# Kernel tuning notes

Hardware: AMD Instinct MI355X
Metric: run time of the kernel (lower is better)

## Reference

```python
import jax, jax.numpy as jnp
import numpy as np

K = 20          # neighbors
EPS = 1e-5      # BatchNorm eps
SLOPE = 0.2     # LeakyReLU negative slope


def setup_inputs() -> dict:
    key = jax.random.key(0)
    k1, k2 = jax.random.split(key)
    B, C, N, O = 8, 64, 4096, 64
    x = jax.random.normal(k1, (B, C, N), dtype=jnp.float32)
    # 1x1 Conv2d(2C -> O, bias=False) kernel, squeezed to (O, 2C)
    W = jax.random.normal(k2, (O, 2 * C), dtype=jnp.float32) * 0.05
    gamma = jnp.ones((O,), jnp.float32)   # BN weight
    beta = jnp.zeros((O,), jnp.float32)   # BN bias
    return {"x": x, "W": W, "gamma": gamma, "beta": beta}


def _edgeconv(x, W, gamma, beta):
    B, C, N = x.shape
    xt = jnp.transpose(x, (0, 2, 1))                       # (B, N, C)
    # KNN on negative squared distance (matches torch topk of -dist)
    xx = jnp.sum(x * x, axis=1)                            # (B, N)
    inner = jnp.einsum('bnc,bmc->bnm', xt, xt)             # (B, N, N)
    neg_dist = 2.0 * inner - xx[:, :, None] - xx[:, None, :]
    _, idx = jax.lax.top_k(neg_dist, K)                    # (B, N, K) int32
    # gather neighbor features: nbr[b,n,k,c] = xt[b, idx[b,n,k], c]
    nbr = xt[jnp.arange(B)[:, None, None], idx]            # (B, N, K, C)
    center = jnp.broadcast_to(xt[:, :, None, :], (B, N, K, C))
    edge = jnp.concatenate([nbr - center, center], axis=-1)  # (B, N, K, 2C)
    # 1x1 conv == channel matmul
    y = jnp.einsum('bnkc,oc->bnko', edge, W)               # (B, N, K, O)
    # BatchNorm2d (training mode: batch statistics over B,N,K per channel)
    mean = jnp.mean(y, axis=(0, 1, 2))
    var = jnp.var(y, axis=(0, 1, 2))
    yn = (y - mean) * jax.lax.rsqrt(var + EPS) * gamma + beta
    ya = jnp.where(yn >= 0, yn, SLOPE * yn)                # LeakyReLU(0.2)
    out = jnp.max(ya, axis=2)                              # max over k -> (B, N, O)
    return jnp.transpose(out, (0, 2, 1))                   # (B, O, N)


def reference(x, W, gamma, beta):
    return _edgeconv(x, W, gamma, beta)
```

## Files before the change

### kernel.cpp

```cpp
#include <hip/hip_runtime.h>
#include <hip/hip_bf16.h>
#include <math.h>

#define B 8
#define C 64
#define NN 4096
#define O 64
#define KNN 20

typedef float f32x4 __attribute__((ext_vector_type(4)));
typedef short short8_t __attribute__((ext_vector_type(8)));

__device__ inline uint32_t fkey(float f) {
    uint32_t u = __float_as_uint(f);
    return u ^ (((uint32_t)((int32_t)u >> 31)) | 0x80000000u);
}

__device__ inline uint32_t med3u(uint32_t a, uint32_t b, uint32_t c) {
    uint32_t r;
    asm("v_med3_u32 %0, %1, %2, %3" : "=v"(r) : "v"(a), "v"(b), "v"(c));
    return r;
}
__device__ inline uint32_t umax(uint32_t a, uint32_t b) { return a > b ? a : b; }

__device__ inline uint32_t maxall16(uint32_t v) {
    uint32_t t;
    t = (uint32_t)__builtin_amdgcn_update_dpp(0, (int)v, 0x140, 0xF, 0xF, true);
    v = umax(v, t);
    t = (uint32_t)__builtin_amdgcn_update_dpp(0, (int)v, 0x141, 0xF, 0xF, true);
    v = umax(v, t);
    t = (uint32_t)__builtin_amdgcn_update_dpp(0, (int)v, 0x4E, 0xF, 0xF, true);
    v = umax(v, t);
    t = (uint32_t)__builtin_amdgcn_update_dpp(0, (int)v, 0xB1, 0xF, 0xF, true);
    v = umax(v, t);
    return v;
}

__global__ __launch_bounds__(256) void k1_split(const float* __restrict__ x,
                                                float* __restrict__ xt,
                                                __hip_bfloat16* __restrict__ xh,
                                                float* __restrict__ xx) {
    __shared__ float tile[64][65];
    int b  = blockIdx.x / (NN / 64);
    int n0 = (blockIdx.x % (NN / 64)) * 64;
    int t = threadIdx.x;
    #pragma unroll
    for (int it = 0; it < 16; ++it) {
        int i = it * 256 + t;
        int c = i >> 6, n = i & 63;
        tile[c][n] = x[(size_t)b * C * NN + (size_t)c * NN + n0 + n];
    }
    __syncthreads();
    #pragma unroll
    for (int it = 0; it < 16; ++it) {
        int i = it * 256 + t;
        int n = i >> 6, c = i & 63;
        float v = tile[c][n];
        size_t off = ((size_t)(b * NN + n0 + n)) * C + c;
        xt[off] = v;
        xh[off] = __float2bfloat16(v);
    }
    if (t < 64) {
        float s = 0.f;
        #pragma unroll
        for (int c = 0; c < 64; ++c) { float v = tile[c][t]; s = fmaf(v, v, s); }
        xx[(size_t)b * NN + t + n0] = s;
    }
}

__global__ __launch_bounds__(256) void k2_knn(const __hip_bfloat16* __restrict__ xh,
                                              const float* __restrict__ xt,
                                              const float* __restrict__ xx,
                                              int* __restrict__ idx) {
    int b  = blockIdx.x & 7;
    int n0 = (blockIdx.x >> 3) << 4;
    int t = threadIdx.x;
    int w = t >> 6, lane = t & 63;
    int laneid = lane & 15, grp = lane >> 4;

    const __hip_bfloat16* xhb = xh + (size_t)b * NN * 64;
    const float* xxb = xx + (size_t)b * NN;
    const float* xtb = xt + (size_t)b * NN * 64;

    size_t qoff = (size_t)(n0 + laneid) * 64 + grp * 8;
    short8_t Ah0 = *(const short8_t*)(xhb + qoff);
    short8_t Ah1 = *(const short8_t*)(xhb + qoff + 32);

    uint32_t qq[4][12];
    #pragma unroll
    for (int j = 0; j < 4; ++j)
        #pragma unroll
        for (int i = 0; i < 12; ++i) qq[j][i] = 0;

    int cand0 = w * 1024 + laneid;
    {
        const __hip_bfloat16* p0 = xhb + (size_t)cand0 * 64 + grp * 8;
        short8_t nB0 = *(const short8_t*)p0;
        short8_t nB1 = *(const short8_t*)(p0 + 32);
        float nxx = xxb[cand0];
        #pragma unroll 4
        for (int tt = 0; tt < 64; ++tt) {
            short8_t B0 = nB0, B1 = nB1;
            float xxc = nxx;
            int ci = cand0 + tt * 16;
            {
                const __hip_bfloat16* np = xhb + (size_t)(ci + 16) * 64 + grp * 8;
                nB0 = *(const short8_t*)np;
                nB1 = *(const short8_t*)(np + 32);
                nxx = xxb[ci + 16];
            }
            f32x4 acc = {0.f, 0.f, 0.f, 0.f};
            acc = __builtin_amdgcn_mfma_f32_16x16x32_bf16(Ah0, B0, acc, 0, 0, 0);
            acc = __builtin_amdgcn_mfma_f32_16x16x32_bf16(Ah1, B1, acc, 0, 0, 0);
            uint32_t invcol = 4095u - (uint32_t)ci;
            #pragma unroll
            for (int j = 0; j < 4; ++j) {
                uint32_t nv = (fkey(fmaf(acc[j], 2.f, -xxc)) & 0xFFFFF000u) | invcol;
                #pragma unroll
                for (int i = 11; i >= 1; --i)
                    qq[j][i] = med3u(qq[j][i - 1], qq[j][i], nv);
                qq[j][0] = umax(qq[j][0], nv);
            }
        }
    }

    __shared__ uint32_t mbuf[16][4][20];
    __shared__ uint32_t cand[16][32];
    __shared__ uint32_t rkk[16][32];
    __shared__ float qrow[16][64];

    #pragma unroll
    for (int i = 0; i < 4; ++i) {
        int e = i * 256 + t;
        int r = e >> 6, cc = e & 63;
        qrow[r][cc] = xtb[(size_t)(n0 + r) * 64 + cc];
    }

    #pragma unroll 1
    for (int r = 0; r < 20; ++r) {
        #pragma unroll
        for (int j = 0; j < 4; ++j) {
            uint32_t bk = maxall16(qq[j][0]);
            bool win = (qq[j][0] == bk);
            #pragma unroll
            for (int i = 0; i < 11; ++i) qq[j][i] = win ? qq[j][i + 1] : qq[j][i];
            qq[j][11] = win ? 0u : qq[j][11];
            if (laneid == 0) mbuf[grp * 4 + j][w][r] = bk;
        }
    }
    __syncthreads();

    {
        int q = w * 4 + grp;
        const uint32_t* mb = &mbuf[q][0][0];
        uint32_t e0 = mb[laneid],      e1 = mb[16 + laneid], e2 = mb[32 + laneid],
                 e3 = mb[48 + laneid], e4 = mb[64 + laneid];
        #pragma unroll 1
        for (int r = 0; r < 32; ++r) {
            uint32_t bk = umax(umax(umax(e0, e1), umax(e2, e3)), e4);
            bk = maxall16(bk);
            e0 = (e0 == bk) ? 0u : e0;
            e1 = (e1 == bk) ? 0u : e1;
            e2 = (e2 == bk) ? 0u : e2;
            e3 = (e3 == bk) ? 0u : e3;
            e4 = (e4 == bk) ? 0u : e4;
            if (laneid == 0) cand[q][r] = 4095u - (bk & 4095u);
        }
    }
    __syncthreads();

    int rq = t >> 4, rs = t & 15;
    float qxx = xxb[n0 + rq];
    const float4* qr = (const float4*)qrow[rq];
    uint32_t mycol[2], mykey[2];
    #pragma unroll
    for (int e = 0; e < 2; ++e) {
        uint32_t col = cand[rq][rs + 16 * e];
        const float4* cr = (const float4*)(xtb + (size_t)col * 64);
        float a = 0.f;
        #pragma unroll
        for (int i = 0; i < 16; ++i) {
            float4 qv = qr[i], cv = cr[i];
            a = fmaf(qv.x, cv.x, a); a = fmaf(qv.y, cv.y, a);
            a = fmaf(qv.z, cv.z, a); a = fmaf(qv.w, cv.w, a);
        }
        float d = 2.f * a - qxx - xxb[col];
        mycol[e] = col;
        mykey[e] = fkey(d);
        rkk[rq][rs + 16 * e] = mykey[e];
    }
    __syncthreads();
    size_t ob = ((size_t)(b * NN) + n0 + rq) * KNN;
    #pragma unroll
    for (int e = 0; e < 2; ++e) {
        uint32_t ke = mykey[e], ce = mycol[e];
        int rank = 0;
        #pragma unroll
        for (int jj = 0; jj < 32; ++jj) {
            uint32_t kj = rkk[rq][jj], cj = cand[rq][jj];
            rank += (kj > ke || (kj == ke && cj < ce)) ? 1 : 0;
        }
        if (rank < KNN) idx[ob + rank] = (int)ce;
    }
}

__global__ __launch_bounds__(256) void k3a_gemm(const float* __restrict__ xt,
                                                const float* __restrict__ W,
                                                float* __restrict__ Z,
                                                float* __restrict__ Z2) {
    __shared__ float W0t[64][65];
    __shared__ float W21t[64][65];
    __shared__ float xs[16][64];
    int t = threadIdx.x;
    #pragma unroll
    for (int it = 0; it < 16; ++it) {
        int i = it * 256 + t;
        int o = i >> 6, c = i & 63;
        float w0 = W[o * 128 + c];
        float w1 = W[o * 128 + 64 + c];
        W0t[c][o]  = w0;
        W21t[c][o] = w1 - w0;
    }
    int b  = blockIdx.x / (NN / 16);
    int nb = (blockIdx.x % (NN / 16)) * 16;
    #pragma unroll
    for (int it = 0; it < 4; ++it) {
        int i = it * 256 + t;
        int r = i >> 6, c = i & 63;
        xs[r][c] = xt[((size_t)(b * NN + nb + r)) * C + c];
    }
    __syncthreads();
    int o = t & 63, rg = t >> 6;
    #pragma unroll
    for (int rr = 0; rr < 4; ++rr) {
        int r = rg * 4 + rr;
        float z = 0.f, z2 = 0.f;
        #pragma unroll
        for (int c = 0; c < 64; ++c) {
            float xv = xs[r][c];
            z  = fmaf(xv, W0t[c][o],  z);
            z2 = fmaf(xv, W21t[c][o], z2);
        }
        size_t off = ((size_t)(b * NN + nb + r)) * 64 + o;
        Z[off]  = z;
        Z2[off] = z2;
    }
}

__global__ __launch_bounds__(256) void k3b_gather(const float* __restrict__ Z,
                                                  const float* __restrict__ Z2,
                                                  const int* __restrict__ idx,
                                                  float* __restrict__ maxY,
                                                  float* __restrict__ minY,
                                                  float* __restrict__ partials) {
    int t = threadIdx.x;
    int p = t >> 6, o = t & 63;
    int b = blockIdx.x & 7;
    int n = (blockIdx.x >> 3) * 4 + p;
    size_t base = (size_t)(b * NN + n);
    float z2 = Z2[base * 64 + o];
    __shared__ int sidx[4][KNN];
    if (o < KNN) sidx[p][o] = idx[base * KNN + o];
    __syncthreads();
    const float* Zb = Z + (size_t)b * NN * 64;
    float s1 = 0.f, s2 = 0.f, mx = -INFINITY, mn = INFINITY;
    #pragma unroll
    for (int k = 0; k < KNN; ++k) {
        float y = Zb[(size_t)sidx[p][k] * 64 + o] + z2;
        s1 += y;
        s2 = fmaf(y, y, s2);
        mx = fmaxf(mx, y);
        mn = fminf(mn, y);
    }
    maxY[base * 64 + o] = mx;
    minY[base * 64 + o] = mn;
    __shared__ float red[2][4][64];
    red[0][p][o] = s1;
    red[1][p][o] = s2;
    __syncthreads();
    if (t < 64) {
        float a = red[0][0][t] + red[0][1][t] + red[0][2][t] + red[0][3][t];
        float c = red[1][0][t] + red[1][1][t] + red[1][2][t] + red[1][3][t];
        partials[(size_t)blockIdx.x * 128 + t]      = a;
        partials[(size_t)blockIdx.x * 128 + 64 + t] = c;
    }
}

__global__ __launch_bounds__(256) void k4a_reduce(const float* __restrict__ partials,
                                                  float* __restrict__ partials2) {
    int g = blockIdx.x;
    int t = threadIdx.x;
    int col = t & 127, half = t >> 7;
    float s = 0.f;
    for (int r = half; r < 128; r += 2)
        s += partials[((size_t)g * 128 + r) * 128 + col];
    __shared__ float red[2][128];
    red[half][col] = s;
    __syncthreads();
    if (t < 128) partials2[(size_t)g * 128 + t] = red[0][t] + red[1][t];
}

__global__ __launch_bounds__(128) void k4b_stats(const float* __restrict__ partials2,
                                                 const float* __restrict__ gamma,
                                                 const float* __restrict__ beta,
                                                 float* __restrict__ ss) {
    int t = threadIdx.x;
    double s = 0.0;
    for (int i = 0; i < 64; ++i)
        s += (double)partials2[(size_t)i * 128 + t];
    __shared__ double red[128];
    red[t] = s;
    __syncthreads();
    if (t < 64) {
        double a = red[t], c = red[64 + t];
        double M = (double)B * NN * KNN;
        double mean = a / M;
        double var  = c / M - mean * mean;
        float sc = gamma[t] * rsqrtf((float)var + 1e-5f);
        float sh = beta[t] - (float)mean * sc;
        ss[t]      = sc;
        ss[64 + t] = sh;
    }
}

__global__ __launch_bounds__(256) void k5_out(const float* __restrict__ maxY,
                                              const float* __restrict__ minY,
                                              const float* __restrict__ ss,
                                              float* __restrict__ out) {
    __shared__ float tile[64][65];
    __shared__ float sc[64], sh[64];
    int t = threadIdx.x;
    if (t < 64) { sc[t] = ss[t]; sh[t] = ss[64 + t]; }
    int b  = blockIdx.x / (NN / 64);
    int n0 = (blockIdx.x % (NN / 64)) * 64;
    __syncthreads();
    #pragma unroll
    for (int it = 0; it < 16; ++it) {
        int i = it * 256 + t;
        int nl = i >> 6, o = i & 63;
        size_t off = ((size_t)(b * NN + n0 + nl)) * 64 + o;
        float s = sc[o];
        float v = (s >= 0.f) ? maxY[off] : minY[off];
        v = fmaf(v, s, sh[o]);
        v = (v >= 0.f) ? v : 0.2f * v;
        tile[nl][o] = v;
    }
    __syncthreads();
    #pragma unroll
    for (int it = 0; it < 16; ++it) {
        int i = it * 256 + t;
        int o = i >> 6, nl = i & 63;
        out[((size_t)(b * O + o)) * NN + n0 + nl] = tile[nl][o];
    }
}

extern "C" void kernel_launch(void* const* d_in, const int* in_sizes, int n_in,
                              void* d_out, int out_size, void* d_ws, size_t ws_size,
                              hipStream_t stream) {
    const float* x     = (const float*)d_in[0];
    const float* W     = (const float*)d_in[1];
    const float* gamma = (const float*)d_in[2];
    const float* beta  = (const float*)d_in[3];
    float* out = (float*)d_out;

    float* ws = (float*)d_ws;
    float* xx = ws;
    float* xt = xx + (size_t)B * NN;
    __hip_bfloat16* xh = (__hip_bfloat16*)(xt + (size_t)B * NN * C);
    int*   idx = (int*)(xh + (size_t)B * NN * C);
    float* Z   = (float*)(idx + (size_t)B * NN * KNN);
    float* Z2  = Z + (size_t)B * NN * O;
    float* maxY = Z2 + (size_t)B * NN * O;
    float* minY = maxY + (size_t)B * NN * O;
    float* partials  = minY + (size_t)B * NN * O;
    float* partials2 = partials + (size_t)(B * NN / 4) * 128;
    float* ss = partials2 + 64 * 128;

    k1_split<<<B * (NN / 64), 256, 0, stream>>>(x, xt, xh, xx);
    k2_knn<<<B * (NN / 16), 256, 0, stream>>>(xh, xt, xx, idx);
    k3a_gemm<<<B * (NN / 16), 256, 0, stream>>>(xt, W, Z, Z2);
    k3b_gather<<<B * (NN / 4), 256, 0, stream>>>(Z, Z2, idx, maxY, minY, partials);
    k4a_reduce<<<64, 256, 0, stream>>>(partials, partials2);
    k4b_stats<<<1, 128, 0, stream>>>(partials2, gamma, beta, ss);
    k5_out<<<B * (NN / 64), 256, 0, stream>>>(maxY, minY, ss, out);
}
```

Measured before the change: 254.0 us.

## Simplify KNN selection: min-queue on raw float bits, drop merge stage, rerank 80 candidates

The per-lane top-k queue now keeps 10 entries instead of 12. Keys are built as raw float bits of (−2 − xx_q + 2·dot − xx_c), which are always negative, so a min on unsigned bits picks the largest distance without the fkey transform. The shared-memory merge of per-wave candidates to 32 is removed. All 80 per-wave candidates are instead reranked exactly in fp32 and selected with a 20-round max reduction, which removes one sync and the rank-counting pass. Exactness rests on each wave's true neighbors fitting in a 10-deep per-lane queue, and on the bq offset keeping every key negative.

Measured after the change: 383.8 us. 1.51x slower.

```diff
diff --git a/kernel.cpp b/kernel.cpp
--- a/kernel.cpp
+++ b/kernel.cpp
@@ -22,6 +22,7 @@
     return r;
 }
 __device__ inline uint32_t umax(uint32_t a, uint32_t b) { return a > b ? a : b; }
+__device__ inline uint32_t umin(uint32_t a, uint32_t b) { return a < b ? a : b; }
 
 __device__ inline uint32_t maxall16(uint32_t v) {
     uint32_t t;
@@ -35,6 +36,18 @@
     v = umax(v, t);
     return v;
 }
+__device__ inline uint32_t minall16(uint32_t v) {
+    uint32_t t;
+    t = (uint32_t)__builtin_amdgcn_update_dpp(0, (int)v, 0x140, 0xF, 0xF, true);
+    v = umin(v, t);
+    t = (uint32_t)__builtin_amdgcn_update_dpp(0, (int)v, 0x141, 0xF, 0xF, true);
+    v = umin(v, t);
+    t = (uint32_t)__builtin_amdgcn_update_dpp(0, (int)v, 0x4E, 0xF, 0xF, true);
+    v = umin(v, t);
+    t = (uint32_t)__builtin_amdgcn_update_dpp(0, (int)v, 0xB1, 0xF, 0xF, true);
+    v = umin(v, t);
+    return v;
+}
 
 __global__ __launch_bounds__(256) void k1_split(const float* __restrict__ x,
                                                 float* __restrict__ xt,
@@ -86,11 +99,15 @@
     short8_t Ah0 = *(const short8_t*)(xhb + qoff);
     short8_t Ah1 = *(const short8_t*)(xhb + qoff + 32);
 
-    uint32_t qq[4][12];
+    float bq[4];
+    #pragma unroll
+    for (int j = 0; j < 4; ++j) bq[j] = -2.f - xxb[n0 + grp * 4 + j];
+
+    uint32_t qq[4][10];
     #pragma unroll
     for (int j = 0; j < 4; ++j)
         #pragma unroll
-        for (int i = 0; i < 12; ++i) qq[j][i] = 0;
+        for (int i = 0; i < 10; ++i) qq[j][i] = 0xFFFFFFFFu;
 
     int cand0 = w * 1024 + laneid;
     {
@@ -112,22 +129,20 @@
             f32x4 acc = {0.f, 0.f, 0.f, 0.f};
             acc = __builtin_amdgcn_mfma_f32_16x16x32_bf16(Ah0, B0, acc, 0, 0, 0);
             acc = __builtin_amdgcn_mfma_f32_16x16x32_bf16(Ah1, B1, acc, 0, 0, 0);
-            uint32_t invcol = 4095u - (uint32_t)ci;
             #pragma unroll
             for (int j = 0; j < 4; ++j) {
-                uint32_t nv = (fkey(fmaf(acc[j], 2.f, -xxc)) & 0xFFFFF000u) | invcol;
+                uint32_t u = __float_as_uint(fmaf(acc[j], 2.f, bq[j] - xxc));
+                uint32_t nv = (u & 0xFFFFF000u) | (uint32_t)ci;
                 #pragma unroll
-                for (int i = 11; i >= 1; --i)
+                for (int i = 9; i >= 1; --i)
                     qq[j][i] = med3u(qq[j][i - 1], qq[j][i], nv);
-                qq[j][0] = umax(qq[j][0], nv);
+                qq[j][0] = umin(qq[j][0], nv);
             }
         }
     }
 
-    __shared__ uint32_t mbuf[16][4][20];
-    __shared__ uint32_t cand[16][32];
-    __shared__ uint32_t rkk[16][32];
-    __shared__ float qrow[16][64];
+    __shared__ uint32_t cand[16][84];
+    __shared__ float qrow[16][68];
 
     #pragma unroll
     for (int i = 0; i < 4; ++i) {
@@ -140,31 +155,12 @@
     for (int r = 0; r < 20; ++r) {
         #pragma unroll
         for (int j = 0; j < 4; ++j) {
-            uint32_t bk = maxall16(qq[j][0]);
+            uint32_t bk = minall16(qq[j][0]);
             bool win = (qq[j][0] == bk);
             #pragma unroll
-            for (int i = 0; i < 11; ++i) qq[j][i] = win ? qq[j][i + 1] : qq[j][i];
-            qq[j][11] = win ? 0u : qq[j][11];
-            if (laneid == 0) mbuf[grp * 4 + j][w][r] = bk;
-        }
-    }
-    __syncthreads();
-
-    {
-        int q = w * 4 + grp;
-        const uint32_t* mb = &mbuf[q][0][0];
-        uint32_t e0 = mb[laneid],      e1 = mb[16 + laneid], e2 = mb[32 + laneid],
-                 e3 = mb[48 + laneid], e4 = mb[64 + laneid];
-        #pragma unroll 1
-        for (int r = 0; r < 32; ++r) {
-            uint32_t bk = umax(umax(umax(e0, e1), umax(e2, e3)), e4);
-            bk = maxall16(bk);
-            e0 = (e0 == bk) ? 0u : e0;
-            e1 = (e1 == bk) ? 0u : e1;
-            e2 = (e2 == bk) ? 0u : e2;
-            e3 = (e3 == bk) ? 0u : e3;
-            e4 = (e4 == bk) ? 0u : e4;
-            if (laneid == 0) cand[q][r] = 4095u - (bk & 4095u);
+            for (int i = 0; i < 9; ++i) qq[j][i] = win ? qq[j][i + 1] : qq[j][i];
+            qq[j][9] = win ? 0xFFFFFFFFu : qq[j][9];
+            if (laneid == 0) cand[grp * 4 + j][w * 20 + r] = bk & 4095u;
         }
     }
     __syncthreads();
@@ -172,9 +168,9 @@
     int rq = t >> 4, rs = t & 15;
     float qxx = xxb[n0 + rq];
     const float4* qr = (const float4*)qrow[rq];
-    uint32_t mycol[2], mykey[2];
-    #pragma unroll
-    for (int e = 0; e < 2; ++e) {
+    uint32_t ky[5], cl[5];
+    #pragma unroll
+    for (int e = 0; e < 5; ++e) {
         uint32_t col = cand[rq][rs + 16 * e];
         const float4* cr = (const float4*)(xtb + (size_t)col * 64);
         float a = 0.f;
@@ -185,22 +181,36 @@
             a = fmaf(qv.z, cv.z, a); a = fmaf(qv.w, cv.w, a);
         }
         float d = 2.f * a - qxx - xxb[col];
-        mycol[e] = col;
-        mykey[e] = fkey(d);
-        rkk[rq][rs + 16 * e] = mykey[e];
-    }
-    __syncthreads();
+        ky[e] = fkey(d);
+        cl[e] = col;
+    }
+
     size_t ob = ((size_t)(b * NN) + n0 + rq) * KNN;
-    #pragma unroll
-    for (int e = 0; e < 2; ++e) {
-        uint32_t ke = mykey[e], ce = mycol[e];
-        int rank = 0;
-        #pragma unroll
-        for (int jj = 0; jj < 32; ++jj) {
-            uint32_t kj = rkk[rq][jj], cj = cand[rq][jj];
-            rank += (kj > ke || (kj == ke && cj < ce)) ? 1 : 0;
-        }
-        if (rank < KNN) idx[ob + rank] = (int)ce;
+    int rowsh = lane & 48;
+    #pragma unroll 1
+    for (int r = 0; r < KNN; ++r) {
+        uint32_t bl = umax(umax(umax(ky[0], ky[1]), umax(ky[2], ky[3])), ky[4]);
+        uint32_t bg = maxall16(bl);
+        bool m0 = (ky[0] == bg), m1 = (ky[1] == bg), m2 = (ky[2] == bg),
+             m3 = (ky[3] == bg), m4 = (ky[4] == bg);
+        bool any = m0 | m1 | m2 | m3 | m4;
+        unsigned long long bal = __ballot(any);
+        uint32_t rowbits = (uint32_t)((bal >> rowsh) & 0xFFFFull);
+        int firstl = __builtin_ctz(rowbits);
+        if (laneid == firstl) {
+            bool c0 = m0;
+            bool c1 = m1 && !m0;
+            bool c2 = m2 && !(m0 | m1);
+            bool c3 = m3 && !(m0 | m1 | m2);
+            bool c4 = m4 && !(m0 | m1 | m2 | m3);
+            uint32_t c = c0 ? cl[0] : (c1 ? cl[1] : (c2 ? cl[2] : (c3 ? cl[3] : cl[4])));
+            idx[ob + r] = (int)c;
+            ky[0] = c0 ? 0u : ky[0];
+            ky[1] = c1 ? 0u : ky[1];
+            ky[2] = c2 ? 0u : ky[2];
+            ky[3] = c3 ? 0u : ky[3];
+            ky[4] = c4 ? 0u : ky[4];
+        }
     }
 }
 
```
